# Optimization experiments

Measured on AMD Instinct MI355X. Metric: run time of the kernel, lower is better.

## Reference

```python
import jax, jax.numpy as jnp
import numpy as np

N, E, D_IN, D_H, D_OUT = 50000, 800000, 128, 128, 40
EPS = 1e-5


def setup_inputs() -> dict:
    key = jax.random.key(0)
    ks = jax.random.split(key, 12)
    x = jax.random.normal(ks[0], (N, D_IN), dtype=jnp.float32)
    edge_index = jax.random.randint(ks[1], (2, E), 0, N, dtype=jnp.int32)
    s = 1.0 / np.sqrt(D_H)
    return {
        "x": x,
        "edge_index": edge_index,
        "W1": jax.random.normal(ks[2], (D_IN, D_H), jnp.float32) * s,
        "b1": jnp.zeros((D_H,), jnp.float32),
        "W2": jax.random.normal(ks[3], (D_H, D_H), jnp.float32) * s,
        "b2": jnp.zeros((D_H,), jnp.float32),
        "g1": jnp.ones((D_H,), jnp.float32),
        "be1": jnp.zeros((D_H,), jnp.float32),
        "g2": jnp.ones((D_H,), jnp.float32),
        "be2": jnp.zeros((D_H,), jnp.float32),
        "g3": jnp.ones((D_H,), jnp.float32),
        "be3": jnp.zeros((D_H,), jnp.float32),
        "Wm": jax.random.normal(ks[4], (D_H, D_OUT), jnp.float32) * s,
        "bm": jnp.zeros((D_OUT,), jnp.float32),
    }


def _gcn_conv(x, W, b, src, dst, dinv):
    # GCNConv: x' = D^{-1/2}(A+I)D^{-1/2} (x W) + b
    xw = x @ W                                   # [N, H]
    coef = dinv[src] * dinv[dst]                 # [E]
    agg = jax.ops.segment_sum(xw[src] * coef[:, None], dst, num_segments=x.shape[0])
    agg = agg + xw * (dinv * dinv)[:, None]      # self-loop term
    return agg + b


def _bn(x, g, b):
    # BatchNorm1d in training mode: biased batch statistics over nodes
    m = jnp.mean(x, axis=0)
    v = jnp.var(x, axis=0)
    return g * (x - m) * jax.lax.rsqrt(v + EPS) + b


def reference(x, edge_index, W1, b1, W2, b2, g1, be1, g2, be2, g3, be3, Wm, bm):
    src, dst = edge_index[0], edge_index[1]
    # degree with self-loops (GCN symmetric normalization, computed on dst/col)
    deg = 1.0 + jax.ops.segment_sum(jnp.ones((E,), jnp.float32), dst, num_segments=N)
    dinv = jax.lax.rsqrt(deg)
    h = _gcn_conv(x, W1, b1, src, dst, dinv)
    h = jax.nn.relu(_bn(h, g1, be1))            # dropout is identity in eval
    h = _gcn_conv(h, W2, b2, src, dst, dinv)
    h = jax.nn.relu(_bn(h, g2, be2))
    h = _bn(h, g3, be3)
    h = h @ Wm + bm
    return jax.nn.log_softmax(h, axis=1)
```

## Files before the change

### kernel.cpp

```cpp
#include <hip/hip_runtime.h>
#include <hip/hip_fp16.h>
#include <math.h>

#define BN_EPS 1e-5f
#define CAP 128

typedef __attribute__((ext_vector_type(8))) short short8;
typedef __attribute__((ext_vector_type(4))) float floatx4;

__device__ inline unsigned short f2bf(float f) {
    union { float f; unsigned u; } x; x.f = f;
    unsigned r = x.u + 0x7fff + ((x.u >> 16) & 1);
    return (unsigned short)(r >> 16);
}
__device__ inline float bf2f(unsigned short h) {
    union { float f; unsigned u; } x; x.u = ((unsigned)h) << 16; return x.f;
}

__device__ inline void bn_sc_sh(float sum, float sumsq, float g, float be, float invN,
                                float& sc, float& sh) {
    float mean = sum * invN;
    float var = sumsq * invN - mean * mean;
    sc = g * rsqrtf(var + BN_EPS);
    sh = be - mean * sc;
}

__device__ inline void pack_one(int idx, const float* W1, const float* W2, const float* Wm,
                                unsigned short* p1, unsigned short* p2, unsigned short* pm) {
    const float* W;
    unsigned short* pack;
    int f, l = idx & 63, t, n, stride, ncols;
    if (idx < 2048) {
        W = W1; pack = p1; f = idx >> 6; t = f >> 3; n = (f & 7) * 16 + (l & 15);
        stride = 128; ncols = 128;
    } else if (idx < 4096) {
        W = W2; pack = p2; f = (idx - 2048) >> 6; t = f >> 3; n = (f & 7) * 16 + (l & 15);
        stride = 128; ncols = 128;
    } else {
        W = Wm; pack = pm; f = (idx - 4096) >> 6; t = f / 3; n = (f % 3) * 16 + (l & 15);
        stride = 40; ncols = 40;
    }
    int q = l >> 4;
    unsigned short* pp = pack + f * 1024 + l * 16;
#pragma unroll
    for (int j = 0; j < 8; ++j) {
        int k = t * 32 + q * 8 + j;
        float v = (n < ncols) ? W[k * stride + n] : 0.f;
        unsigned short hi = f2bf(v);
        float lo = v - bf2f(hi);
        pp[j] = hi;
        pp[8 + j] = f2bf(lo);
    }
}

__global__ __launch_bounds__(256) void k_pre(const float* __restrict__ W1,
                                             const float* __restrict__ W2,
                                             const float* __restrict__ Wm,
                                             unsigned short* __restrict__ p1,
                                             unsigned short* __restrict__ p2,
                                             unsigned short* __restrict__ pm,
                                             int4* __restrict__ zdst, int nz4) {
    if (blockIdx.x < 19) {
        int idx = blockIdx.x * 256 + threadIdx.x;
        if (idx < 4864) pack_one(idx, W1, W2, Wm, p1, p2, pm);
        return;
    }
    int i = (blockIdx.x - 19) * 256 + threadIdx.x;
    if (i < nz4) zdst[i] = make_int4(0, 0, 0, 0);
}

__device__ inline void load_row8(const float* arow, int kbase, float av[8]) {
    float4 a0 = *(const float4*)(arow + kbase);
    float4 a1 = *(const float4*)(arow + kbase + 4);
    av[0] = a0.x; av[1] = a0.y; av[2] = a0.z; av[3] = a0.w;
    av[4] = a1.x; av[5] = a1.y; av[6] = a1.z; av[7] = a1.w;
}
__device__ inline void load_row8(const __half* arow, int kbase, float av[8]) {
    float4 raw = *(const float4*)(arow + kbase);
    const __half2* h = (const __half2*)&raw;
#pragma unroll
    for (int i = 0; i < 4; ++i) {
        float2 f = __half22float2(h[i]);
        av[2 * i] = f.x;
        av[2 * i + 1] = f.y;
    }
}

template <typename T, bool FUSE_BN>
__device__ __forceinline__ void gemm_body(int bid, const T* __restrict__ A,
                                          const unsigned short* __restrict__ packW,
                                          const float* __restrict__ sums,
                                          const float* __restrict__ g,
                                          const float* __restrict__ be, float invN,
                                          __half* __restrict__ C16, int M) {
    int lane = threadIdx.x & 63;
    int wv = threadIdx.x >> 6;
    int m0 = (bid * 4 + wv) * 16;
    if (m0 >= M) return;
    int row = lane & 15, quad = lane >> 4;

    floatx4 acc[8];
#pragma unroll
    for (int nt = 0; nt < 8; ++nt) acc[nt] = (floatx4){0.f, 0.f, 0.f, 0.f};

    const T* arow = A + (size_t)(m0 + row) * 128;

    float av[4][8];
#pragma unroll
    for (int t = 0; t < 4; ++t) load_row8(arow, t * 32 + quad * 8, av[t]);

#pragma unroll
    for (int t = 0; t < 4; ++t) {
        int kbase = t * 32 + quad * 8;
        if (FUSE_BN) {
#pragma unroll
            for (int j = 0; j < 8; ++j) {
                int c = kbase + j;
                float sc, sh;
                bn_sc_sh(sums[c], sums[128 + c], g[c], be[c], invN, sc, sh);
                av[t][j] = fmaxf(av[t][j] * sc + sh, 0.f);
            }
        }
        short8 ah, al;
#pragma unroll
        for (int j = 0; j < 8; ++j) {
            unsigned short hi = f2bf(av[t][j]);
            ah[j] = (short)hi;
            al[j] = (short)f2bf(av[t][j] - bf2f(hi));
        }
        const unsigned short* wp = packW + (size_t)(t * 8) * 1024 + lane * 16;
#pragma unroll
        for (int nt = 0; nt < 8; ++nt) {
            short8 wh = *(const short8*)wp;
            short8 wl = *(const short8*)(wp + 8);
            wp += 1024;
            acc[nt] = __builtin_amdgcn_mfma_f32_16x16x32_bf16(ah, wh, acc[nt], 0, 0, 0);
            acc[nt] = __builtin_amdgcn_mfma_f32_16x16x32_bf16(al, wh, acc[nt], 0, 0, 0);
            acc[nt] = __builtin_amdgcn_mfma_f32_16x16x32_bf16(ah, wl, acc[nt], 0, 0, 0);
        }
    }

#pragma unroll
    for (int nt = 0; nt < 8; ++nt) {
#pragma unroll
        for (int r = 0; r < 4; ++r) {
            C16[(size_t)(m0 + quad * 4 + r) * 128 + nt * 16 + row] =
                __float2half_rn(acc[nt][r]);
        }
    }
}

__device__ __forceinline__ void fill_body(int b, const int* __restrict__ src,
                                          const int* __restrict__ dst, int E,
                                          int* __restrict__ fillc,
                                          unsigned short* __restrict__ col16, int nfill) {
    int g = b & 7;
    int rank = b >> 3;
    int stride = (nfill >> 3) * 256;
    for (int e = rank * 256 + threadIdx.x; e < E; e += stride) {
        int d = dst[e];
        if ((d & 7) != g) continue;
        int r = atomicAdd(&fillc[d], 1);
        if (r < CAP) col16[(size_t)d * CAP + r] = (unsigned short)src[e];
    }
}

__global__ __launch_bounds__(256) void k_fill_gemm1(const float* __restrict__ x,
                                                    const unsigned short* __restrict__ packW1,
                                                    __half* __restrict__ y16, int M, int ngemm,
                                                    const int* __restrict__ src,
                                                    const int* __restrict__ dst, int E,
                                                    int* __restrict__ fillc,
                                                    unsigned short* __restrict__ col16,
                                                    int nfill) {
    int bid = (int)blockIdx.x;
    int chunk = bid >> 4;
    int pos = bid & 15;
    if (pos < 8) {
        int u = chunk * 8 + pos;
        if (u < ngemm)
            gemm_body<float, false>(u, x, packW1, nullptr, nullptr, nullptr, 0.f, y16, M);
        return;
    }
    int b = chunk * 8 + (pos - 8);
    if (b < nfill) fill_body(b, src, dst, E, fillc, col16, nfill);
}

template <typename T, bool FUSE_BN>
__global__ __launch_bounds__(256) void k_gemm(const T* __restrict__ A,
                                              const unsigned short* __restrict__ packW,
                                              const float* __restrict__ sums,
                                              const float* __restrict__ g,
                                              const float* __restrict__ be, float invN,
                                              __half* __restrict__ C16, int M) {
    gemm_body<T, FUSE_BN>(blockIdx.x, A, packW, sums, g, be, invN, C16, M);
}

__global__ __launch_bounds__(256) void k_gather(const __half2* __restrict__ y16,
                                                const int* __restrict__ fillc,
                                                const unsigned short* __restrict__ col16,
                                                const float* __restrict__ bias,
                                                __half2* __restrict__ out, int N) {
    int wv = threadIdx.x >> 6;
    int lane = threadIdx.x & 63;
    int n = blockIdx.x * 4 + wv;
    if (n >= N) return;
    int degraw = fillc[n];
    float dn = rsqrtf(1.f + (float)degraw);
    float2 self = __half22float2(y16[(size_t)n * 64 + lane]);
    float2 acc;
    acc.x = dn * self.x;
    acc.y = dn * self.y;
    int deg = min(degraw, CAP);
    const unsigned short* cb = col16 + (size_t)n * CAP;
    for (int jb = 0; jb < deg; jb += 64) {
        int cnt = min(64, deg - jb);
        int idx = (lane < cnt) ? (int)cb[jb + lane] : 0;
        float dv = (lane < cnt) ? rsqrtf(1.f + (float)fillc[idx]) : 0.f;
        int jj = 0;
        for (; jj + 8 <= cnt; jj += 8) {
            int s0 = __shfl(idx, jj + 0, 64);
            int s1 = __shfl(idx, jj + 1, 64);
            int s2 = __shfl(idx, jj + 2, 64);
            int s3 = __shfl(idx, jj + 3, 64);
            int s4 = __shfl(idx, jj + 4, 64);
            int s5 = __shfl(idx, jj + 5, 64);
            int s6 = __shfl(idx, jj + 6, 64);
            int s7 = __shfl(idx, jj + 7, 64);
            float w0 = __shfl(dv, jj + 0, 64);
            float w1 = __shfl(dv, jj + 1, 64);
            float w2 = __shfl(dv, jj + 2, 64);
            float w3 = __shfl(dv, jj + 3, 64);
            float w4 = __shfl(dv, jj + 4, 64);
            float w5 = __shfl(dv, jj + 5, 64);
            float w6 = __shfl(dv, jj + 6, 64);
            float w7 = __shfl(dv, jj + 7, 64);
            float2 r0 = __half22float2(y16[(size_t)s0 * 64 + lane]);
            float2 r1 = __half22float2(y16[(size_t)s1 * 64 + lane]);
            float2 r2 = __half22float2(y16[(size_t)s2 * 64 + lane]);
            float2 r3 = __half22float2(y16[(size_t)s3 * 64 + lane]);
            float2 r4 = __half22float2(y16[(size_t)s4 * 64 + lane]);
            float2 r5 = __half22float2(y16[(size_t)s5 * 64 + lane]);
            float2 r6 = __half22float2(y16[(size_t)s6 * 64 + lane]);
            float2 r7 = __half22float2(y16[(size_t)s7 * 64 + lane]);
            acc.x += w0 * r0.x + w1 * r1.x + w2 * r2.x + w3 * r3.x +
                     w4 * r4.x + w5 * r5.x + w6 * r6.x + w7 * r7.x;
            acc.y += w0 * r0.y + w1 * r1.y + w2 * r2.y + w3 * r3.y +
                     w4 * r4.y + w5 * r5.y + w6 * r6.y + w7 * r7.y;
        }
        for (; jj < cnt; ++jj) {
            int s = __shfl(idx, jj, 64);
            float w = __shfl(dv, jj, 64);
            float2 r = __half22float2(y16[(size_t)s * 64 + lane]);
            acc.x += w * r.x;
            acc.y += w * r.y;
        }
    }
    float2 b = *(const float2*)&bias[lane << 1];
    float2 o;
    o.x = dn * acc.x + b.x;
    o.y = dn * acc.y + b.y;
    out[(size_t)n * 64 + lane] = __float22half2_rn(o);
}

template <bool TRANSFORM>
__global__ __launch_bounds__(256) void k_stats(const __half2* __restrict__ h, int N,
                                               const float* __restrict__ sums2,
                                               const float* __restrict__ g2,
                                               const float* __restrict__ be2, float invN,
                                               float* __restrict__ stats) {
    int cp = threadIdx.x & 63;
    int rg = threadIdx.x >> 6;
    int rbeg = blockIdx.x * 256;
    int rend = min(rbeg + 256, N);
    float scx = 1.f, shx = 0.f, scy = 1.f, shy = 0.f;
    if (TRANSFORM) {
        int c = cp * 2;
        bn_sc_sh(sums2[c], sums2[128 + c], g2[c], be2[c], invN, scx, shx);
        bn_sc_sh(sums2[c + 1], sums2[128 + c + 1], g2[c + 1], be2[c + 1], invN, scy, shy);
    }
    float sx = 0.f, sy = 0.f, s2x = 0.f, s2y = 0.f;
    for (int r = rbeg + rg; r < rend; r += 4) {
        float2 v = __half22float2(h[(size_t)r * 64 + cp]);
        if (TRANSFORM) {
            v.x = fmaxf(v.x * scx + shx, 0.f);
            v.y = fmaxf(v.y * scy + shy, 0.f);
        }
        sx += v.x; sy += v.y;
        s2x += v.x * v.x; s2y += v.y * v.y;
    }
    __shared__ float ls[4][256];
    ls[0][threadIdx.x] = sx;
    ls[1][threadIdx.x] = sy;
    ls[2][threadIdx.x] = s2x;
    ls[3][threadIdx.x] = s2y;
    __syncthreads();
    if (threadIdx.x < 64) {
        int t = threadIdx.x;
        float a0 = ls[0][t] + ls[0][t + 64] + ls[0][t + 128] + ls[0][t + 192];
        float a1 = ls[1][t] + ls[1][t + 64] + ls[1][t + 128] + ls[1][t + 192];
        float a2 = ls[2][t] + ls[2][t + 64] + ls[2][t + 128] + ls[2][t + 192];
        float a3 = ls[3][t] + ls[3][t + 64] + ls[3][t + 128] + ls[3][t + 192];
        atomicAdd(&stats[2 * t], a0);
        atomicAdd(&stats[2 * t + 1], a1);
        atomicAdd(&stats[128 + 2 * t], a2);
        atomicAdd(&stats[128 + 2 * t + 1], a3);
    }
}

__global__ __launch_bounds__(256) void k_final(const __half* __restrict__ h,
                                               const float* __restrict__ sums2,
                                               const float* __restrict__ g2,
                                               const float* __restrict__ be2,
                                               const float* __restrict__ sums3,
                                               const float* __restrict__ g3,
                                               const float* __restrict__ be3, float invN,
                                               const unsigned short* __restrict__ packWm,
                                               const float* __restrict__ bm,
                                               float* __restrict__ out, int N) {
    int lane = threadIdx.x & 63;
    int wv = threadIdx.x >> 6;
    int m0 = (blockIdx.x * 4 + wv) * 16;
    if (m0 >= N) return;
    int row = lane & 15, quad = lane >> 4;

    floatx4 acc[3];
#pragma unroll
    for (int nt = 0; nt < 3; ++nt) acc[nt] = (floatx4){0.f, 0.f, 0.f, 0.f};

    const __half* arow = h + (size_t)(m0 + row) * 128;

    float av[4][8];
#pragma unroll
    for (int t = 0; t < 4; ++t) load_row8(arow, t * 32 + quad * 8, av[t]);

#pragma unroll
    for (int t = 0; t < 4; ++t) {
        int kbase = t * 32 + quad * 8;
#pragma unroll
        for (int j = 0; j < 8; ++j) {
            int c = kbase + j;
            float sc2, sh2, sc3, sh3;
            bn_sc_sh(sums2[c], sums2[128 + c], g2[c], be2[c], invN, sc2, sh2);
            bn_sc_sh(sums3[c], sums3[128 + c], g3[c], be3[c], invN, sc3, sh3);
            av[t][j] = fmaxf(av[t][j] * sc2 + sh2, 0.f) * sc3 + sh3;
        }
        short8 ah, al;
#pragma unroll
        for (int j = 0; j < 8; ++j) {
            unsigned short hi = f2bf(av[t][j]);
            ah[j] = (short)hi;
            al[j] = (short)f2bf(av[t][j] - bf2f(hi));
        }
        const unsigned short* wp = packWm + (size_t)(t * 3) * 1024 + lane * 16;
#pragma unroll
        for (int nt = 0; nt < 3; ++nt) {
            short8 wh = *(const short8*)wp;
            short8 wl = *(const short8*)(wp + 8);
            wp += 1024;
            acc[nt] = __builtin_amdgcn_mfma_f32_16x16x32_bf16(ah, wh, acc[nt], 0, 0, 0);
            acc[nt] = __builtin_amdgcn_mfma_f32_16x16x32_bf16(al, wh, acc[nt], 0, 0, 0);
            acc[nt] = __builtin_amdgcn_mfma_f32_16x16x32_bf16(ah, wl, acc[nt], 0, 0, 0);
        }
    }

    float bb[3];
#pragma unroll
    for (int nt = 0; nt < 3; ++nt) {
        int col = nt * 16 + row;
        bb[nt] = (col < 40) ? bm[col] : 0.f;
    }
    bool val2 = (row < 8);

#pragma unroll
    for (int r = 0; r < 4; ++r) {
        int m = m0 + quad * 4 + r;
        float v0 = acc[0][r] + bb[0];
        float v1 = acc[1][r] + bb[1];
        float v2 = acc[2][r] + bb[2];
        float mx = fmaxf(v0, v1);
        if (val2) mx = fmaxf(mx, v2);
#pragma unroll
        for (int off = 1; off <= 8; off <<= 1) mx = fmaxf(mx, __shfl_xor(mx, off, 64));
        float s = expf(v0 - mx) + expf(v1 - mx) + (val2 ? expf(v2 - mx) : 0.f);
#pragma unroll
        for (int off = 1; off <= 8; off <<= 1) s += __shfl_xor(s, off, 64);
        float lse = mx + logf(s);
        if (m < N) {
            out[(size_t)m * 40 + row] = v0 - lse;
            out[(size_t)m * 40 + 16 + row] = v1 - lse;
            if (val2) out[(size_t)m * 40 + 32 + row] = v2 - lse;
        }
    }
}

extern "C" void kernel_launch(void* const* d_in, const int* in_sizes, int n_in,
                              void* d_out, int out_size, void* d_ws, size_t ws_size,
                              hipStream_t stream) {
    const float* x   = (const float*)d_in[0];
    const int*   ei  = (const int*)d_in[1];
    const float* W1  = (const float*)d_in[2];
    const float* b1  = (const float*)d_in[3];
    const float* W2  = (const float*)d_in[4];
    const float* b2  = (const float*)d_in[5];
    const float* g1  = (const float*)d_in[6];
    const float* be1 = (const float*)d_in[7];
    const float* g2  = (const float*)d_in[8];
    const float* be2 = (const float*)d_in[9];
    const float* g3  = (const float*)d_in[10];
    const float* be3 = (const float*)d_in[11];
    const float* Wm  = (const float*)d_in[12];
    const float* bm  = (const float*)d_in[13];
    float* out = (float*)d_out;

    int N = in_sizes[0] / 128;
    int E = in_sizes[1] / 2;
    const int* srcs = ei;
    const int* dsts = ei + E;
    float invN = 1.0f / (float)N;

    char* ws = (char*)d_ws;
    size_t off = 0;
    auto alloc = [&](size_t bytes) -> void* {
        void* p = ws + off;
        off += (bytes + 255) & ~(size_t)255;
        return p;
    };
    size_t fill_rounded = (((size_t)N * 4) + 255) & ~(size_t)255;
    int*   fillc   = (int*)alloc((size_t)N * 4);
    float* statsAll= (float*)alloc(3 * 256 * 4);
    float* stats1  = statsAll;
    float* stats2  = statsAll + 256;
    float* stats3  = statsAll + 512;
    unsigned short* col16 = (unsigned short*)alloc((size_t)N * CAP * 2);
    unsigned short* packW1 = (unsigned short*)alloc(32768 * 2);
    unsigned short* packW2 = (unsigned short*)alloc(32768 * 2);
    unsigned short* packWm = (unsigned short*)alloc(12288 * 2);
    __half* y16 = (__half*)alloc((size_t)N * 128 * 2);
    __half* h16 = (__half*)alloc((size_t)N * 128 * 2);
    (void)ws_size; (void)n_in; (void)out_size;

    int nthb = (N + 255) / 256;
    int gatherb = (N + 3) / 4;
    int gfb = (N + 63) / 64;
    int ngemm = (N + 63) / 64;
    const int NFILL = 1024;

    int nz4 = (int)((fill_rounded + 3 * 256 * 4) / 16);
    int zb = (nz4 + 255) / 256;

    k_pre<<<19 + zb, 256, 0, stream>>>(W1, W2, Wm, packW1, packW2, packWm,
                                       (int4*)fillc, nz4);

    int nchunk = 128;
    k_fill_gemm1<<<nchunk * 16, 256, 0, stream>>>(x, packW1, y16, N, ngemm, srcs, dsts, E,
                                                  fillc, col16, NFILL);

    k_gather<<<gatherb, 256, 0, stream>>>((const __half2*)y16, fillc, col16, b1,
                                          (__half2*)h16, N);
    k_stats<false><<<nthb, 256, 0, stream>>>((const __half2*)h16, N, nullptr, nullptr, nullptr,
                                             invN, stats1);

    k_gemm<__half, true><<<ngemm, 256, 0, stream>>>(h16, packW2, stats1, g1, be1, invN,
                                                    y16, N);
    k_gather<<<gatherb, 256, 0, stream>>>((const __half2*)y16, fillc, col16, b2,
                                          (__half2*)h16, N);
    k_stats<false><<<nthb, 256, 0, stream>>>((const __half2*)h16, N, nullptr, nullptr, nullptr,
                                             invN, stats2);

    k_stats<true><<<nthb, 256, 0, stream>>>((const __half2*)h16, N, stats2, g2, be2, invN,
                                            stats3);
    k_final<<<gfb, 256, 0, stream>>>(h16, stats2, g2, be2, stats3, g3, be3, invN, packWm, bm,
                                     out, N);
}
```

Measured before the change: 327.8 us.

## Fuse BN statistics into gather kernel, split fill and first GEMM launches

Batch-norm statistics for the two GCN layers are now accumulated inside a persistent, grid-strided gather kernel, which removes two separate passes that re-read the aggregated features. The earlier combined fill+GEMM1 kernel is split back into separate fill and GEMM launches, and the fill grid grows from 1024 to 8192 blocks. The last statistics pass gets smaller 64-row blocks for more parallelism. In exchange, the gather loses some occupancy flexibility with a fixed 2048-block grid, and fill and GEMM1 no longer overlap.

```diff
diff --git a/kernel.cpp b/kernel.cpp
--- a/kernel.cpp
+++ b/kernel.cpp
@@ -69,91 +69,11 @@
     if (i < nz4) zdst[i] = make_int4(0, 0, 0, 0);
 }
 
-__device__ inline void load_row8(const float* arow, int kbase, float av[8]) {
-    float4 a0 = *(const float4*)(arow + kbase);
-    float4 a1 = *(const float4*)(arow + kbase + 4);
-    av[0] = a0.x; av[1] = a0.y; av[2] = a0.z; av[3] = a0.w;
-    av[4] = a1.x; av[5] = a1.y; av[6] = a1.z; av[7] = a1.w;
-}
-__device__ inline void load_row8(const __half* arow, int kbase, float av[8]) {
-    float4 raw = *(const float4*)(arow + kbase);
-    const __half2* h = (const __half2*)&raw;
-#pragma unroll
-    for (int i = 0; i < 4; ++i) {
-        float2 f = __half22float2(h[i]);
-        av[2 * i] = f.x;
-        av[2 * i + 1] = f.y;
-    }
-}
-
-template <typename T, bool FUSE_BN>
-__device__ __forceinline__ void gemm_body(int bid, const T* __restrict__ A,
-                                          const unsigned short* __restrict__ packW,
-                                          const float* __restrict__ sums,
-                                          const float* __restrict__ g,
-                                          const float* __restrict__ be, float invN,
-                                          __half* __restrict__ C16, int M) {
-    int lane = threadIdx.x & 63;
-    int wv = threadIdx.x >> 6;
-    int m0 = (bid * 4 + wv) * 16;
-    if (m0 >= M) return;
-    int row = lane & 15, quad = lane >> 4;
-
-    floatx4 acc[8];
-#pragma unroll
-    for (int nt = 0; nt < 8; ++nt) acc[nt] = (floatx4){0.f, 0.f, 0.f, 0.f};
-
-    const T* arow = A + (size_t)(m0 + row) * 128;
-
-    float av[4][8];
-#pragma unroll
-    for (int t = 0; t < 4; ++t) load_row8(arow, t * 32 + quad * 8, av[t]);
-
-#pragma unroll
-    for (int t = 0; t < 4; ++t) {
-        int kbase = t * 32 + quad * 8;
-        if (FUSE_BN) {
-#pragma unroll
-            for (int j = 0; j < 8; ++j) {
-                int c = kbase + j;
-                float sc, sh;
-                bn_sc_sh(sums[c], sums[128 + c], g[c], be[c], invN, sc, sh);
-                av[t][j] = fmaxf(av[t][j] * sc + sh, 0.f);
-            }
-        }
-        short8 ah, al;
-#pragma unroll
-        for (int j = 0; j < 8; ++j) {
-            unsigned short hi = f2bf(av[t][j]);
-            ah[j] = (short)hi;
-            al[j] = (short)f2bf(av[t][j] - bf2f(hi));
-        }
-        const unsigned short* wp = packW + (size_t)(t * 8) * 1024 + lane * 16;
-#pragma unroll
-        for (int nt = 0; nt < 8; ++nt) {
-            short8 wh = *(const short8*)wp;
-            short8 wl = *(const short8*)(wp + 8);
-            wp += 1024;
-            acc[nt] = __builtin_amdgcn_mfma_f32_16x16x32_bf16(ah, wh, acc[nt], 0, 0, 0);
-            acc[nt] = __builtin_amdgcn_mfma_f32_16x16x32_bf16(al, wh, acc[nt], 0, 0, 0);
-            acc[nt] = __builtin_amdgcn_mfma_f32_16x16x32_bf16(ah, wl, acc[nt], 0, 0, 0);
-        }
-    }
-
-#pragma unroll
-    for (int nt = 0; nt < 8; ++nt) {
-#pragma unroll
-        for (int r = 0; r < 4; ++r) {
-            C16[(size_t)(m0 + quad * 4 + r) * 128 + nt * 16 + row] =
-                __float2half_rn(acc[nt][r]);
-        }
-    }
-}
-
-__device__ __forceinline__ void fill_body(int b, const int* __restrict__ src,
-                                          const int* __restrict__ dst, int E,
-                                          int* __restrict__ fillc,
-                                          unsigned short* __restrict__ col16, int nfill) {
+__global__ __launch_bounds__(256) void k_fill(const int* __restrict__ src,
+                                              const int* __restrict__ dst, int E,
+                                              int* __restrict__ fillc,
+                                              unsigned short* __restrict__ col16, int nfill) {
+    int b = (int)blockIdx.x;
     int g = b & 7;
     int rank = b >> 3;
     int stride = (nfill >> 3) * 256;
@@ -165,25 +85,21 @@
     }
 }
 
-__global__ __launch_bounds__(256) void k_fill_gemm1(const float* __restrict__ x,
-                                                    const unsigned short* __restrict__ packW1,
-                                                    __half* __restrict__ y16, int M, int ngemm,
-                                                    const int* __restrict__ src,
-                                                    const int* __restrict__ dst, int E,
-                                                    int* __restrict__ fillc,
-                                                    unsigned short* __restrict__ col16,
-                                                    int nfill) {
-    int bid = (int)blockIdx.x;
-    int chunk = bid >> 4;
-    int pos = bid & 15;
-    if (pos < 8) {
-        int u = chunk * 8 + pos;
-        if (u < ngemm)
-            gemm_body<float, false>(u, x, packW1, nullptr, nullptr, nullptr, 0.f, y16, M);
-        return;
-    }
-    int b = chunk * 8 + (pos - 8);
-    if (b < nfill) fill_body(b, src, dst, E, fillc, col16, nfill);
+__device__ inline void load_row8(const float* arow, int kbase, float av[8]) {
+    float4 a0 = *(const float4*)(arow + kbase);
+    float4 a1 = *(const float4*)(arow + kbase + 4);
+    av[0] = a0.x; av[1] = a0.y; av[2] = a0.z; av[3] = a0.w;
+    av[4] = a1.x; av[5] = a1.y; av[6] = a1.z; av[7] = a1.w;
+}
+__device__ inline void load_row8(const __half* arow, int kbase, float av[8]) {
+    float4 raw = *(const float4*)(arow + kbase);
+    const __half2* h = (const __half2*)&raw;
+#pragma unroll
+    for (int i = 0; i < 4; ++i) {
+        float2 f = __half22float2(h[i]);
+        av[2 * i] = f.x;
+        av[2 * i + 1] = f.y;
+    }
 }
 
 template <typename T, bool FUSE_BN>
@@ -193,102 +109,137 @@
                                               const float* __restrict__ g,
                                               const float* __restrict__ be, float invN,
                                               __half* __restrict__ C16, int M) {
-    gemm_body<T, FUSE_BN>(blockIdx.x, A, packW, sums, g, be, invN, C16, M);
-}
-
-__global__ __launch_bounds__(256) void k_gather(const __half2* __restrict__ y16,
-                                                const int* __restrict__ fillc,
-                                                const unsigned short* __restrict__ col16,
-                                                const float* __restrict__ bias,
-                                                __half2* __restrict__ out, int N) {
+    int lane = threadIdx.x & 63;
+    int wv = threadIdx.x >> 6;
+    int m0 = ((int)blockIdx.x * 4 + wv) * 16;
+    if (m0 >= M) return;
+    int row = lane & 15, quad = lane >> 4;
+
+    floatx4 acc[8];
+#pragma unroll
+    for (int nt = 0; nt < 8; ++nt) acc[nt] = (floatx4){0.f, 0.f, 0.f, 0.f};
+
+    const T* arow = A + (size_t)(m0 + row) * 128;
+
+    float av[4][8];
+#pragma unroll
+    for (int t = 0; t < 4; ++t) load_row8(arow, t * 32 + quad * 8, av[t]);
+
+#pragma unroll
+    for (int t = 0; t < 4; ++t) {
+        int kbase = t * 32 + quad * 8;
+        if (FUSE_BN) {
+#pragma unroll
+            for (int j = 0; j < 8; ++j) {
+                int c = kbase + j;
+                float sc, sh;
+                bn_sc_sh(sums[c], sums[128 + c], g[c], be[c], invN, sc, sh);
+                av[t][j] = fmaxf(av[t][j] * sc + sh, 0.f);
+            }
+        }
+        short8 ah, al;
+#pragma unroll
+        for (int j = 0; j < 8; ++j) {
+            unsigned short hi = f2bf(av[t][j]);
+            ah[j] = (short)hi;
+            al[j] = (short)f2bf(av[t][j] - bf2f(hi));
+        }
+        const unsigned short* wp = packW + (size_t)(t * 8) * 1024 + lane * 16;
+#pragma unroll
+        for (int nt = 0; nt < 8; ++nt) {
+            short8 wh = *(const short8*)wp;
+            short8 wl = *(const short8*)(wp + 8);
+            wp += 1024;
+            acc[nt] = __builtin_amdgcn_mfma_f32_16x16x32_bf16(ah, wh, acc[nt], 0, 0, 0);
+            acc[nt] = __builtin_amdgcn_mfma_f32_16x16x32_bf16(al, wh, acc[nt], 0, 0, 0);
+            acc[nt] = __builtin_amdgcn_mfma_f32_16x16x32_bf16(ah, wl, acc[nt], 0, 0, 0);
+        }
+    }
+
+#pragma unroll
+    for (int nt = 0; nt < 8; ++nt) {
+#pragma unroll
+        for (int r = 0; r < 4; ++r) {
+            C16[(size_t)(m0 + quad * 4 + r) * 128 + nt * 16 + row] =
+                __float2half_rn(acc[nt][r]);
+        }
+    }
+}
+
+__global__ __launch_bounds__(256) void k_gather_stats(const __half2* __restrict__ y16,
+                                                      const int* __restrict__ fillc,
+                                                      const unsigned short* __restrict__ col16,
+                                                      const float* __restrict__ bias,
+                                                      __half2* __restrict__ out, int N,
+                                                      float* __restrict__ stats) {
     int wv = threadIdx.x >> 6;
     int lane = threadIdx.x & 63;
-    int n = blockIdx.x * 4 + wv;
-    if (n >= N) return;
-    int degraw = fillc[n];
-    float dn = rsqrtf(1.f + (float)degraw);
-    float2 self = __half22float2(y16[(size_t)n * 64 + lane]);
-    float2 acc;
-    acc.x = dn * self.x;
-    acc.y = dn * self.y;
-    int deg = min(degraw, CAP);
-    const unsigned short* cb = col16 + (size_t)n * CAP;
-    for (int jb = 0; jb < deg; jb += 64) {
-        int cnt = min(64, deg - jb);
-        int idx = (lane < cnt) ? (int)cb[jb + lane] : 0;
-        float dv = (lane < cnt) ? rsqrtf(1.f + (float)fillc[idx]) : 0.f;
-        int jj = 0;
-        for (; jj + 8 <= cnt; jj += 8) {
-            int s0 = __shfl(idx, jj + 0, 64);
-            int s1 = __shfl(idx, jj + 1, 64);
-            int s2 = __shfl(idx, jj + 2, 64);
-            int s3 = __shfl(idx, jj + 3, 64);
-            int s4 = __shfl(idx, jj + 4, 64);
-            int s5 = __shfl(idx, jj + 5, 64);
-            int s6 = __shfl(idx, jj + 6, 64);
-            int s7 = __shfl(idx, jj + 7, 64);
-            float w0 = __shfl(dv, jj + 0, 64);
-            float w1 = __shfl(dv, jj + 1, 64);
-            float w2 = __shfl(dv, jj + 2, 64);
-            float w3 = __shfl(dv, jj + 3, 64);
-            float w4 = __shfl(dv, jj + 4, 64);
-            float w5 = __shfl(dv, jj + 5, 64);
-            float w6 = __shfl(dv, jj + 6, 64);
-            float w7 = __shfl(dv, jj + 7, 64);
-            float2 r0 = __half22float2(y16[(size_t)s0 * 64 + lane]);
-            float2 r1 = __half22float2(y16[(size_t)s1 * 64 + lane]);
-            float2 r2 = __half22float2(y16[(size_t)s2 * 64 + lane]);
-            float2 r3 = __half22float2(y16[(size_t)s3 * 64 + lane]);
-            float2 r4 = __half22float2(y16[(size_t)s4 * 64 + lane]);
-            float2 r5 = __half22float2(y16[(size_t)s5 * 64 + lane]);
-            float2 r6 = __half22float2(y16[(size_t)s6 * 64 + lane]);
-            float2 r7 = __half22float2(y16[(size_t)s7 * 64 + lane]);
-            acc.x += w0 * r0.x + w1 * r1.x + w2 * r2.x + w3 * r3.x +
-                     w4 * r4.x + w5 * r5.x + w6 * r6.x + w7 * r7.x;
-            acc.y += w0 * r0.y + w1 * r1.y + w2 * r2.y + w3 * r3.y +
-                     w4 * r4.y + w5 * r5.y + w6 * r6.y + w7 * r7.y;
-        }
-        for (; jj < cnt; ++jj) {
-            int s = __shfl(idx, jj, 64);
-            float w = __shfl(dv, jj, 64);
-            float2 r = __half22float2(y16[(size_t)s * 64 + lane]);
-            acc.x += w * r.x;
-            acc.y += w * r.y;
-        }
-    }
+    int nwave = (int)gridDim.x * 4;
     float2 b = *(const float2*)&bias[lane << 1];
-    float2 o;
-    o.x = dn * acc.x + b.x;
-    o.y = dn * acc.y + b.y;
-    out[(size_t)n * 64 + lane] = __float22half2_rn(o);
-}
-
-template <bool TRANSFORM>
-__global__ __launch_bounds__(256) void k_stats(const __half2* __restrict__ h, int N,
-                                               const float* __restrict__ sums2,
-                                               const float* __restrict__ g2,
-                                               const float* __restrict__ be2, float invN,
-                                               float* __restrict__ stats) {
-    int cp = threadIdx.x & 63;
-    int rg = threadIdx.x >> 6;
-    int rbeg = blockIdx.x * 256;
-    int rend = min(rbeg + 256, N);
-    float scx = 1.f, shx = 0.f, scy = 1.f, shy = 0.f;
-    if (TRANSFORM) {
-        int c = cp * 2;
-        bn_sc_sh(sums2[c], sums2[128 + c], g2[c], be2[c], invN, scx, shx);
-        bn_sc_sh(sums2[c + 1], sums2[128 + c + 1], g2[c + 1], be2[c + 1], invN, scy, shy);
-    }
     float sx = 0.f, sy = 0.f, s2x = 0.f, s2y = 0.f;
-    for (int r = rbeg + rg; r < rend; r += 4) {
-        float2 v = __half22float2(h[(size_t)r * 64 + cp]);
-        if (TRANSFORM) {
-            v.x = fmaxf(v.x * scx + shx, 0.f);
-            v.y = fmaxf(v.y * scy + shy, 0.f);
-        }
+
+    for (int n = (int)blockIdx.x * 4 + wv; n < N; n += nwave) {
+        int degraw = fillc[n];
+        float dn = rsqrtf(1.f + (float)degraw);
+        float2 self = __half22float2(y16[(size_t)n * 64 + lane]);
+        float2 acc;
+        acc.x = dn * self.x;
+        acc.y = dn * self.y;
+        int deg = min(degraw, CAP);
+        const unsigned short* cb = col16 + (size_t)n * CAP;
+        for (int jb = 0; jb < deg; jb += 64) {
+            int cnt = min(64, deg - jb);
+            int idx = (lane < cnt) ? (int)cb[jb + lane] : 0;
+            float dv = (lane < cnt) ? rsqrtf(1.f + (float)fillc[idx]) : 0.f;
+            int jj = 0;
+            for (; jj + 8 <= cnt; jj += 8) {
+                int s0 = __shfl(idx, jj + 0, 64);
+                int s1 = __shfl(idx, jj + 1, 64);
+                int s2 = __shfl(idx, jj + 2, 64);
+                int s3 = __shfl(idx, jj + 3, 64);
+                int s4 = __shfl(idx, jj + 4, 64);
+                int s5 = __shfl(idx, jj + 5, 64);
+                int s6 = __shfl(idx, jj + 6, 64);
+                int s7 = __shfl(idx, jj + 7, 64);
+                float w0 = __shfl(dv, jj + 0, 64);
+                float w1 = __shfl(dv, jj + 1, 64);
+                float w2 = __shfl(dv, jj + 2, 64);
+                float w3 = __shfl(dv, jj + 3, 64);
+                float w4 = __shfl(dv, jj + 4, 64);
+                float w5 = __shfl(dv, jj + 5, 64);
+                float w6 = __shfl(dv, jj + 6, 64);
+                float w7 = __shfl(dv, jj + 7, 64);
+                float2 r0 = __half22float2(y16[(size_t)s0 * 64 + lane]);
+                float2 r1 = __half22float2(y16[(size_t)s1 * 64 + lane]);
+                float2 r2 = __half22float2(y16[(size_t)s2 * 64 + lane]);
+                float2 r3 = __half22float2(y16[(size_t)s3 * 64 + lane]);
+                float2 r4 = __half22float2(y16[(size_t)s4 * 64 + lane]);
+                float2 r5 = __half22float2(y16[(size_t)s5 * 64 + lane]);
+                float2 r6 = __half22float2(y16[(size_t)s6 * 64 + lane]);
+                float2 r7 = __half22float2(y16[(size_t)s7 * 64 + lane]);
+                acc.x += w0 * r0.x + w1 * r1.x + w2 * r2.x + w3 * r3.x +
+                         w4 * r4.x + w5 * r5.x + w6 * r6.x + w7 * r7.x;
+                acc.y += w0 * r0.y + w1 * r1.y + w2 * r2.y + w3 * r3.y +
+                         w4 * r4.y + w5 * r5.y + w6 * r6.y + w7 * r7.y;
+            }
+            for (; jj < cnt; ++jj) {
+                int s = __shfl(idx, jj, 64);
+                float w = __shfl(dv, jj, 64);
+                float2 r = __half22float2(y16[(size_t)s * 64 + lane]);
+                acc.x += w * r.x;
+                acc.y += w * r.y;
+            }
+        }
+        float2 o;
+        o.x = dn * acc.x + b.x;
+        o.y = dn * acc.y + b.y;
+        __half2 h2 = __float22half2_rn(o);
+        out[(size_t)n * 64 + lane] = h2;
+        float2 v = __half22float2(h2);
         sx += v.x; sy += v.y;
         s2x += v.x * v.x; s2y += v.y * v.y;
     }
+
     __shared__ float ls[4][256];
     ls[0][threadIdx.x] = sx;
     ls[1][threadIdx.x] = sy;
@@ -308,6 +259,48 @@
     }
 }
 
+__global__ __launch_bounds__(256) void k_stats_t(const __half2* __restrict__ h, int N,
+                                                 const float* __restrict__ sums2,
+                                                 const float* __restrict__ g2,
+                                                 const float* __restrict__ be2, float invN,
+                                                 float* __restrict__ stats) {
+    int cp = threadIdx.x & 63;
+    int rg = threadIdx.x >> 6;
+    int rbeg = blockIdx.x * 64;
+    int rend = min(rbeg + 64, N);
+    float scx, shx, scy, shy;
+    {
+        int c = cp * 2;
+        bn_sc_sh(sums2[c], sums2[128 + c], g2[c], be2[c], invN, scx, shx);
+        bn_sc_sh(sums2[c + 1], sums2[128 + c + 1], g2[c + 1], be2[c + 1], invN, scy, shy);
+    }
+    float sx = 0.f, sy = 0.f, s2x = 0.f, s2y = 0.f;
+    for (int r = rbeg + rg; r < rend; r += 4) {
+        float2 v = __half22float2(h[(size_t)r * 64 + cp]);
+        v.x = fmaxf(v.x * scx + shx, 0.f);
+        v.y = fmaxf(v.y * scy + shy, 0.f);
+        sx += v.x; sy += v.y;
+        s2x += v.x * v.x; s2y += v.y * v.y;
+    }
+    __shared__ float ls[4][256];
+    ls[0][threadIdx.x] = sx;
+    ls[1][threadIdx.x] = sy;
+    ls[2][threadIdx.x] = s2x;
+    ls[3][threadIdx.x] = s2y;
+    __syncthreads();
+    if (threadIdx.x < 64) {
+        int t = threadIdx.x;
+        float a0 = ls[0][t] + ls[0][t + 64] + ls[0][t + 128] + ls[0][t + 192];
+        float a1 = ls[1][t] + ls[1][t + 64] + ls[1][t + 128] + ls[1][t + 192];
+        float a2 = ls[2][t] + ls[2][t + 64] + ls[2][t + 128] + ls[2][t + 192];
+        float a3 = ls[3][t] + ls[3][t + 64] + ls[3][t + 128] + ls[3][t + 192];
+        atomicAdd(&stats[2 * t], a0);
+        atomicAdd(&stats[2 * t + 1], a1);
+        atomicAdd(&stats[128 + 2 * t], a2);
+        atomicAdd(&stats[128 + 2 * t + 1], a3);
+    }
+}
+
 __global__ __launch_bounds__(256) void k_final(const __half* __restrict__ h,
                                                const float* __restrict__ sums2,
                                                const float* __restrict__ g2,
@@ -320,7 +313,7 @@
                                                float* __restrict__ out, int N) {
     int lane = threadIdx.x & 63;
     int wv = threadIdx.x >> 6;
-    int m0 = (blockIdx.x * 4 + wv) * 16;
+    int m0 = ((int)blockIdx.x * 4 + wv) * 16;
     if (m0 >= N) return;
     int row = lane & 15, quad = lane >> 4;
 
@@ -440,11 +433,11 @@
     __half* h16 = (__half*)alloc((size_t)N * 128 * 2);
     (void)ws_size; (void)n_in; (void)out_size;
 
-    int nthb = (N + 255) / 256;
-    int gatherb = (N + 3) / 4;
+    int ngemm = (N + 63) / 64;
     int gfb = (N + 63) / 64;
-    int ngemm = (N + 63) / 64;
-    const int NFILL = 1024;
+    int s3b = (N + 63) / 64;
+    const int NFILL = 8192;
+    const int NGATH = 2048;
 
     int nz4 = (int)((fill_rounded + 3 * 256 * 4) / 16);
     int zb = (nz4 + 255) / 256;
@@ -452,24 +445,20 @@
     k_pre<<<19 + zb, 256, 0, stream>>>(W1, W2, Wm, packW1, packW2, packWm,
                                        (int4*)fillc, nz4);
 
-    int nchunk = 128;
-    k_fill_gemm1<<<nchunk * 16, 256, 0, stream>>>(x, packW1, y16, N, ngemm, srcs, dsts, E,
-                                                  fillc, col16, NFILL);
-
-    k_gather<<<gatherb, 256, 0, stream>>>((const __half2*)y16, fillc, col16, b1,
-                                          (__half2*)h16, N);
-    k_stats<false><<<nthb, 256, 0, stream>>>((const __half2*)h16, N, nullptr, nullptr, nullptr,
-                                             invN, stats1);
+    k_fill<<<NFILL, 256, 0, stream>>>(srcs, dsts, E, fillc, col16, NFILL);
+    k_gemm<float, false><<<ngemm, 256, 0, stream>>>(x, packW1, nullptr, nullptr, nullptr,
+                                                    invN, y16, N);
+
+    k_gather_stats<<<NGATH, 256, 0, stream>>>((const __half2*)y16, fillc, col16, b1,
+                                              (__half2*)h16, N, stats1);
 
     k_gemm<__half, true><<<ngemm, 256, 0, stream>>>(h16, packW2, stats1, g1, be1, invN,
                                                     y16, N);
-    k_gather<<<gatherb, 256, 0, stream>>>((const __half2*)y16, fillc, col16, b2,
-                                          (__half2*)h16, N);
-    k_stats<false><<<nthb, 256, 0, stream>>>((const __half2*)h16, N, nullptr, nullptr, nullptr,
-                                             invN, stats2);
-
-    k_stats<true><<<nthb, 256, 0, stream>>>((const __half2*)h16, N, stats2, g2, be2, invN,
-                                            stats3);
+    k_gather_stats<<<NGATH, 256, 0, stream>>>((const __half2*)y16, fillc, col16, b2,
+                                              (__half2*)h16, N, stats2);
+
+    k_stats_t<<<s3b, 256, 0, stream>>>((const __half2*)h16, N, stats2, g2, be2, invN,
+                                       stats3);
     k_final<<<gfb, 256, 0, stream>>>(h16, stats2, g2, be2, stats3, g3, be3, invN, packWm, bm,
                                      out, N);
 }
```

Result: slower. 483.5 us (+47.5%).
